# Optimization experiments

Measured on AMD Instinct MI355X. Metric: run time of the kernel, lower is better.

## Reference

```python
import jax, jax.numpy as jnp
import numpy as np

H = 1024          # h_dim
FF = 4 * H
E = 8             # num_expert
TOP_K = 2


def setup_inputs() -> dict:
    key = jax.random.key(0)
    ks = jax.random.split(key, 7)
    B, S = 4, 2048
    s = 0.02
    return {
        "x": jax.random.normal(ks[0], (B, S, H), dtype=jnp.float32),
        "Wg": jax.random.normal(ks[1], (H, E), dtype=jnp.float32) * s,
        "bg": jnp.zeros((E,), dtype=jnp.float32),
        "W1": jax.random.normal(ks[2], (E, H, FF), dtype=jnp.float32) * s,
        "b1": jnp.zeros((E, FF), dtype=jnp.float32),
        "W2": jax.random.normal(ks[3], (E, FF, H), dtype=jnp.float32) * s,
        "b2": jnp.zeros((E, H), dtype=jnp.float32),
    }


def _moe(x, Wg, bg, W1, b1, W2, b2):
    B, S, h = x.shape
    hs = x.reshape(-1, h)                                  # [T, H]
    logits = hs @ Wg + bg                                  # [T, E]
    probs = jax.nn.softmax(logits.astype(jnp.float32), axis=-1)
    w, idx = jax.lax.top_k(probs, TOP_K)                   # [T, K]
    w = jax.nn.softmax(w, axis=-1).astype(x.dtype)         # renormalize over top-k
    out = jnp.zeros_like(hs)
    for e in range(E):
        # per-token combine weight for expert e (0 if not selected)
        w_e = jnp.sum(w * (idx == e), axis=-1)             # [T]
        y = jax.nn.relu(hs @ W1[e] + b1[e]) @ W2[e] + b2[e]  # [T, H]
        out = out + w_e[:, None] * y
    return out.reshape(B, S, h), logits


def reference(x, Wg, bg, W1, b1, W2, b2):
    return _moe(x, Wg, bg, W1, b1, W2, b2)
```

## Files before the change

### kernel.cpp

```cpp
#include <hip/hip_runtime.h>
#include <hip/hip_bf16.h>

#define T_TOKENS 8192
#define HD 1024
#define FF 4096
#define NEXP 8
#define NR_MAX 17408

typedef __attribute__((ext_vector_type(8))) short bf16x8;
typedef __attribute__((ext_vector_type(4))) float f32x4;
typedef unsigned short ushort8v __attribute__((ext_vector_type(8)));

static __device__ __forceinline__ float b2f(ushort u) {
    union { unsigned u; float f; } c; c.u = ((unsigned)u) << 16; return c.f;
}
static __device__ __forceinline__ ushort f2b(float f) {
    union { float f; unsigned u; } c; c.f = f;
    unsigned r = c.u + 0x7fffu + ((c.u >> 16) & 1u);
    return (ushort)(r >> 16);
}

__global__ __launch_bounds__(256) void gate_kernel(
    const float* __restrict__ x, const float* __restrict__ Wg, const float* __restrict__ bg,
    float* __restrict__ logits, int* __restrict__ counts,
    int* __restrict__ e0a, int* __restrict__ e1a,
    float* __restrict__ w0a, float* __restrict__ w1a)
{
    int t = blockIdx.x * 4 + (threadIdx.x >> 6);
    int l = threadIdx.x & 63;
    const float* xr = x + (size_t)t * HD;
    float acc[8] = {0,0,0,0,0,0,0,0};
    #pragma unroll
    for (int i = 0; i < 4; ++i) {
        int h0 = i * 256 + l * 4;
        float4 xv = *(const float4*)(xr + h0);
        #pragma unroll
        for (int j = 0; j < 4; ++j) {
            float xs = (&xv.x)[j];
            const float4* wr = (const float4*)(Wg + (size_t)(h0 + j) * NEXP);
            float4 wa = wr[0], wb = wr[1];
            acc[0] = fmaf(xs, wa.x, acc[0]);
            acc[1] = fmaf(xs, wa.y, acc[1]);
            acc[2] = fmaf(xs, wa.z, acc[2]);
            acc[3] = fmaf(xs, wa.w, acc[3]);
            acc[4] = fmaf(xs, wb.x, acc[4]);
            acc[5] = fmaf(xs, wb.y, acc[5]);
            acc[6] = fmaf(xs, wb.z, acc[6]);
            acc[7] = fmaf(xs, wb.w, acc[7]);
        }
    }
    #pragma unroll
    for (int off = 32; off > 0; off >>= 1) {
        #pragma unroll
        for (int e = 0; e < 8; ++e) acc[e] += __shfl_down(acc[e], off, 64);
    }
    if (l == 0) {
        float lg[8];
        #pragma unroll
        for (int e = 0; e < 8; ++e) {
            lg[e] = acc[e] + bg[e];
            logits[(size_t)t * NEXP + e] = lg[e];
        }
        float m = lg[0];
        #pragma unroll
        for (int e = 1; e < 8; ++e) m = fmaxf(m, lg[e]);
        float p[8], s = 0.f;
        #pragma unroll
        for (int e = 0; e < 8; ++e) { p[e] = expf(lg[e] - m); s += p[e]; }
        float inv = 1.f / s;
        #pragma unroll
        for (int e = 0; e < 8; ++e) p[e] *= inv;
        int i0 = 0;
        #pragma unroll
        for (int e = 1; e < 8; ++e) if (p[e] > p[i0]) i0 = e;
        int i1 = (i0 == 0) ? 1 : 0;
        #pragma unroll
        for (int e = 0; e < 8; ++e) if (e != i0 && p[e] > p[i1]) i1 = e;
        float ed = expf(p[i1] - p[i0]);
        float w0 = 1.f / (1.f + ed);
        float w1 = ed / (1.f + ed);
        e0a[t] = i0; e1a[t] = i1; w0a[t] = w0; w1a[t] = w1;
        atomicAdd(&counts[i0], 1);
        atomicAdd(&counts[i1], 1);
    }
}

__global__ void offsets_kernel(const int* __restrict__ counts, int* __restrict__ off) {
    if (threadIdx.x == 0) {
        int o = 0;
        for (int e = 0; e < 8; ++e) { off[e] = o; o += (counts[e] + 127) & ~127; }
        off[8] = o;
    }
}

__global__ __launch_bounds__(256) void assign_kernel(
    const int* __restrict__ e0a, const int* __restrict__ e1a,
    const int* __restrict__ off, int* __restrict__ fill,
    int* __restrict__ row0, int* __restrict__ row1, int* __restrict__ row_token)
{
    int t = blockIdx.x * 256 + threadIdx.x;
    if (t >= T_TOKENS) return;
    int e0 = e0a[t];
    int r0 = off[e0] + atomicAdd(&fill[e0], 1);
    row0[t] = r0; row_token[r0] = t;
    int e1 = e1a[t];
    int r1 = off[e1] + atomicAdd(&fill[e1], 1);
    row1[t] = r1; row_token[r1] = t;
}

__global__ __launch_bounds__(256) void gather_kernel(
    const float* __restrict__ x, const int* __restrict__ row_token, ushort* __restrict__ Xp)
{
    int r = blockIdx.x;
    int tok = row_token[r];
    int c = threadIdx.x * 4;
    ushort4 o;
    if (tok >= 0 && tok < T_TOKENS) {
        float4 v = *(const float4*)(x + (size_t)tok * HD + c);
        o.x = f2b(v.x); o.y = f2b(v.y); o.z = f2b(v.z); o.w = f2b(v.w);
    } else {
        o.x = 0; o.y = 0; o.z = 0; o.w = 0;
    }
    *(ushort4*)(Xp + (size_t)r * HD + c) = o;
}

__global__ __launch_bounds__(256) void transpose_cvt_kernel(
    const float* __restrict__ in, ushort* __restrict__ out, int R, int C)
{
    __shared__ ushort tile[64][65];
    size_t esz = (size_t)R * C;
    const float* ein = in + (size_t)blockIdx.z * esz;
    ushort* eout = out + (size_t)blockIdx.z * esz;
    int c0 = blockIdx.x * 64, r0 = blockIdx.y * 64;
    int tr = threadIdx.x >> 4;
    int tc = (threadIdx.x & 15) * 4;
    #pragma unroll
    for (int i = 0; i < 4; ++i) {
        int r = tr + i * 16;
        float4 v = *(const float4*)(ein + (size_t)(r0 + r) * C + c0 + tc);
        tile[r][tc + 0] = f2b(v.x);
        tile[r][tc + 1] = f2b(v.y);
        tile[r][tc + 2] = f2b(v.z);
        tile[r][tc + 3] = f2b(v.w);
    }
    __syncthreads();
    int twc = threadIdx.x >> 3;
    int twr = (threadIdx.x & 7) * 8;
    #pragma unroll
    for (int i = 0; i < 2; ++i) {
        int cc = twc + i * 32;
        ushort8v v;
        #pragma unroll
        for (int j = 0; j < 8; ++j) v[j] = tile[twr + j][cc];
        *(ushort8v*)(eout + (size_t)(c0 + cc) * R + r0 + twr) = v;
    }
}

template<int K, int NTOT, bool RELU, bool NTSTORE>
__global__ __launch_bounds__(256) void gemm_kernel(
    const ushort* __restrict__ A, const ushort* __restrict__ Bt,
    const float* __restrict__ bias, ushort* __restrict__ Out,
    const int* __restrict__ off)
{
    constexpr int NT = NTOT / 128;
    __shared__ __align__(16) ushort lds[2][2][128 * 32];

    int nwg = gridDim.x;
    int bid = blockIdx.x;
    int wgid = (bid & 7) * (nwg >> 3) + (bid >> 3);
    int ntile = wgid % NT;
    int mtile = wgid / NT;
    int r0 = mtile * 128;
    int total = off[8];
    if (r0 >= total) return;
    int e = 0;
    #pragma unroll
    for (int q = 0; q < 7; ++q) if (r0 >= off[q + 1]) e = q + 1;

    int tid = threadIdx.x;
    int w = tid >> 6, lane = tid & 63;
    int wr = w >> 1, wc = w & 1;
    int lr = lane & 15, lk = lane >> 4;

    const ushort* Ab = A + (size_t)r0 * K;
    const ushort* Bb = Bt + ((size_t)e * NTOT + (size_t)ntile * 128) * K;

    auto stage = [&](const ushort* gbase, ushort* ldsbase) {
        #pragma unroll
        for (int issue = 0; issue < 2; ++issue) {
            int row = issue * 64 + w * 16 + (lane >> 2);
            int chunk = (lane & 3) ^ ((lane >> 3) & 3);
            const ushort* g = gbase + (size_t)row * K + chunk * 8;
            ushort* lp = ldsbase + (issue * 64 + w * 16) * 32;
            __builtin_amdgcn_global_load_lds(
                (const __attribute__((address_space(1))) void*)g,
                (__attribute__((address_space(3))) void*)lp, 16, 0, 0);
        }
    };

    stage(Ab, &lds[0][0][0]);
    stage(Bb, &lds[0][1][0]);

    f32x4 acc[4][4];
    #pragma unroll
    for (int mi = 0; mi < 4; ++mi)
        #pragma unroll
        for (int ni = 0; ni < 4; ++ni) acc[mi][ni] = (f32x4){0.f, 0.f, 0.f, 0.f};

    __syncthreads();

    constexpr int KT = K / 32;
    int cur = 0;
    int slot = lk ^ ((lr >> 1) & 3);
    for (int kt = 0; kt < KT; ++kt) {
        if (kt + 1 < KT) {
            stage(Ab + (kt + 1) * 32, &lds[cur ^ 1][0][0]);
            stage(Bb + (kt + 1) * 32, &lds[cur ^ 1][1][0]);
        }
        const ushort* As = &lds[cur][0][0];
        const ushort* Bs = &lds[cur][1][0];
        bf16x8 a[4], b[4];
        #pragma unroll
        for (int mi = 0; mi < 4; ++mi)
            a[mi] = *(const bf16x8*)(As + (wr * 64 + mi * 16 + lr) * 32 + slot * 8);
        #pragma unroll
        for (int ni = 0; ni < 4; ++ni)
            b[ni] = *(const bf16x8*)(Bs + (wc * 64 + ni * 16 + lr) * 32 + slot * 8);
        #pragma unroll
        for (int mi = 0; mi < 4; ++mi)
            #pragma unroll
            for (int ni = 0; ni < 4; ++ni)
                acc[mi][ni] = __builtin_amdgcn_mfma_f32_16x16x32_bf16(
                    a[mi], b[ni], acc[mi][ni], 0, 0, 0);
        __syncthreads();
        cur ^= 1;
    }

    int c0 = ntile * 128 + wc * 64;
    int rbase = r0 + wr * 64;
    #pragma unroll
    for (int ni = 0; ni < 4; ++ni) {
        int n = c0 + ni * 16 + lr;
        float bv = bias[(size_t)e * NTOT + n];
        #pragma unroll
        for (int mi = 0; mi < 4; ++mi) {
            int m = rbase + mi * 16 + lk * 4;
            #pragma unroll
            for (int j = 0; j < 4; ++j) {
                float v = acc[mi][ni][j] + bv;
                if (RELU) v = fmaxf(v, 0.f);
                ushort* p = &Out[(size_t)(m + j) * NTOT + n];
                if (NTSTORE) __builtin_nontemporal_store(f2b(v), p);
                else *p = f2b(v);
            }
        }
    }
}

__global__ __launch_bounds__(256) void combine_kernel(
    const ushort* __restrict__ Y, const int* __restrict__ row0, const int* __restrict__ row1,
    const float* __restrict__ w0a, const float* __restrict__ w1a, float* __restrict__ out)
{
    int t = blockIdx.x;
    int c = threadIdx.x * 4;
    int r0 = row0[t], r1 = row1[t];
    float w0 = w0a[t], w1 = w1a[t];
    ushort4 ya = *(const ushort4*)(Y + (size_t)r0 * HD + c);
    ushort4 yb = *(const ushort4*)(Y + (size_t)r1 * HD + c);
    float4 o;
    o.x = w0 * b2f(ya.x) + w1 * b2f(yb.x);
    o.y = w0 * b2f(ya.y) + w1 * b2f(yb.y);
    o.z = w0 * b2f(ya.z) + w1 * b2f(yb.z);
    o.w = w0 * b2f(ya.w) + w1 * b2f(yb.w);
    *(float4*)(out + (size_t)t * HD + c) = o;
}

#define WSA(x) (((x) + 255) & ~(size_t)255)
static constexpr size_t OFF_COUNTS = 0;
static constexpr size_t OFF_FILL   = 64;
static constexpr size_t OFF_OFF    = 128;
static constexpr size_t OFF_E0     = 256;
static constexpr size_t OFF_E1     = OFF_E0 + (size_t)T_TOKENS * 4;
static constexpr size_t OFF_W0     = OFF_E1 + (size_t)T_TOKENS * 4;
static constexpr size_t OFF_W1A    = OFF_W0 + (size_t)T_TOKENS * 4;
static constexpr size_t OFF_R0     = OFF_W1A + (size_t)T_TOKENS * 4;
static constexpr size_t OFF_R1     = OFF_R0 + (size_t)T_TOKENS * 4;
static constexpr size_t OFF_RT     = OFF_R1 + (size_t)T_TOKENS * 4;
static constexpr size_t OFF_XP     = WSA(OFF_RT + (size_t)NR_MAX * 4);
static constexpr size_t OFF_W1T    = OFF_XP  + (size_t)NR_MAX * HD * 2;
static constexpr size_t OFF_W2T    = OFF_W1T + (size_t)NEXP * FF * HD * 2;
static constexpr size_t OFF_H1     = OFF_W2T + (size_t)NEXP * HD * FF * 2;
static constexpr size_t OFF_Y      = OFF_H1  + (size_t)NR_MAX * FF * 2;
static constexpr size_t WS_NEEDED  = OFF_Y   + (size_t)NR_MAX * HD * 2;

extern "C" void kernel_launch(void* const* d_in, const int* in_sizes, int n_in,
                              void* d_out, int out_size, void* d_ws, size_t ws_size,
                              hipStream_t stream) {
    (void)in_sizes; (void)n_in; (void)out_size;
    const float* x  = (const float*)d_in[0];
    const float* Wg = (const float*)d_in[1];
    const float* bg = (const float*)d_in[2];
    const float* W1 = (const float*)d_in[3];
    const float* b1 = (const float*)d_in[4];
    const float* W2 = (const float*)d_in[5];
    const float* b2 = (const float*)d_in[6];
    float* out    = (float*)d_out;
    float* logits = out + (size_t)T_TOKENS * HD;

    if (ws_size < WS_NEEDED) return;

    char* ws = (char*)d_ws;
    int*    counts = (int*)(ws + OFF_COUNTS);
    int*    fill   = (int*)(ws + OFF_FILL);
    int*    offp   = (int*)(ws + OFF_OFF);
    int*    e0a    = (int*)(ws + OFF_E0);
    int*    e1a    = (int*)(ws + OFF_E1);
    float*  w0a    = (float*)(ws + OFF_W0);
    float*  w1a    = (float*)(ws + OFF_W1A);
    int*    row0   = (int*)(ws + OFF_R0);
    int*    row1   = (int*)(ws + OFF_R1);
    int*    rowtok = (int*)(ws + OFF_RT);
    ushort* Xp     = (ushort*)(ws + OFF_XP);
    ushort* W1T    = (ushort*)(ws + OFF_W1T);
    ushort* W2T    = (ushort*)(ws + OFF_W2T);
    ushort* H1     = (ushort*)(ws + OFF_H1);
    ushort* Y      = (ushort*)(ws + OFF_Y);

    hipMemsetAsync(ws, 0, 256, stream);
    hipMemsetAsync(rowtok, 0xFF, (size_t)NR_MAX * 4, stream);

    gate_kernel<<<T_TOKENS / 4, 256, 0, stream>>>(x, Wg, bg, logits, counts, e0a, e1a, w0a, w1a);
    offsets_kernel<<<1, 64, 0, stream>>>(counts, offp);
    assign_kernel<<<T_TOKENS / 256, 256, 0, stream>>>(e0a, e1a, offp, fill, row0, row1, rowtok);
    gather_kernel<<<NR_MAX, 256, 0, stream>>>(x, rowtok, Xp);
    transpose_cvt_kernel<<<dim3(FF / 64, HD / 64, NEXP), 256, 0, stream>>>(W1, W1T, HD, FF);
    transpose_cvt_kernel<<<dim3(HD / 64, FF / 64, NEXP), 256, 0, stream>>>(W2, W2T, FF, HD);
    gemm_kernel<HD, FF, true, true>
        <<<(FF / 128) * (NR_MAX / 128), 256, 0, stream>>>(Xp, W1T, b1, H1, offp);
    gemm_kernel<FF, HD, false, false>
        <<<(HD / 128) * (NR_MAX / 128), 256, 0, stream>>>(H1, W2T, b2, Y, offp);
    combine_kernel<<<T_TOKENS, 256, 0, stream>>>(Y, row0, row1, w0a, w1a, out);
}
```

Baseline: 820.4 us.

## Fuse offsets into assign, merge weight transposes, remap GEMM tiles

Folds the single-thread offsets kernel into the assign kernel, which now computes offsets per block in shared memory. It also merges the two weight transpose-convert launches into one, widens the gather to 8 elements per thread, adds an occupancy hint to the GEMM, and uses an M-fast tile mapping for the first GEMM. The nontemporal store on H1 is dropped. Together these aim to cut launch count and improve L2 reuse of the weight tiles, at the cost of a float LDS tile in the transpose (more shared memory) and possibly more register pressure from the launch bound.

Result: faster. 772.5 us (-5.8%).

```diff
diff --git a/kernel.cpp b/kernel.cpp
--- a/kernel.cpp
+++ b/kernel.cpp
@@ -85,19 +85,23 @@
     }
 }
 
-__global__ void offsets_kernel(const int* __restrict__ counts, int* __restrict__ off) {
+__global__ __launch_bounds__(256) void assign_kernel(
+    const int* __restrict__ e0a, const int* __restrict__ e1a,
+    const int* __restrict__ counts, int* __restrict__ fill, int* __restrict__ offg,
+    int* __restrict__ row0, int* __restrict__ row1, int* __restrict__ row_token)
+{
+    __shared__ int off[9];
     if (threadIdx.x == 0) {
         int o = 0;
+        #pragma unroll
         for (int e = 0; e < 8; ++e) { off[e] = o; o += (counts[e] + 127) & ~127; }
         off[8] = o;
-    }
-}
-
-__global__ __launch_bounds__(256) void assign_kernel(
-    const int* __restrict__ e0a, const int* __restrict__ e1a,
-    const int* __restrict__ off, int* __restrict__ fill,
-    int* __restrict__ row0, int* __restrict__ row1, int* __restrict__ row_token)
-{
+        if (blockIdx.x == 0) {
+            #pragma unroll
+            for (int i = 0; i < 9; ++i) offg[i] = off[i];
+        }
+    }
+    __syncthreads();
     int t = blockIdx.x * 256 + threadIdx.x;
     if (t >= T_TOKENS) return;
     int e0 = e0a[t];
@@ -111,53 +115,67 @@
 __global__ __launch_bounds__(256) void gather_kernel(
     const float* __restrict__ x, const int* __restrict__ row_token, ushort* __restrict__ Xp)
 {
-    int r = blockIdx.x;
+    int r = blockIdx.x * 2 + (threadIdx.x >> 7);
+    int c = (threadIdx.x & 127) * 8;
     int tok = row_token[r];
-    int c = threadIdx.x * 4;
-    ushort4 o;
+    ushort8v o;
     if (tok >= 0 && tok < T_TOKENS) {
-        float4 v = *(const float4*)(x + (size_t)tok * HD + c);
-        o.x = f2b(v.x); o.y = f2b(v.y); o.z = f2b(v.z); o.w = f2b(v.w);
+        const float* src = x + (size_t)tok * HD + c;
+        float4 v1 = *(const float4*)(src);
+        float4 v2 = *(const float4*)(src + 4);
+        o[0] = f2b(v1.x); o[1] = f2b(v1.y); o[2] = f2b(v1.z); o[3] = f2b(v1.w);
+        o[4] = f2b(v2.x); o[5] = f2b(v2.y); o[6] = f2b(v2.z); o[7] = f2b(v2.w);
     } else {
-        o.x = 0; o.y = 0; o.z = 0; o.w = 0;
-    }
-    *(ushort4*)(Xp + (size_t)r * HD + c) = o;
-}
-
-__global__ __launch_bounds__(256) void transpose_cvt_kernel(
-    const float* __restrict__ in, ushort* __restrict__ out, int R, int C)
-{
-    __shared__ ushort tile[64][65];
-    size_t esz = (size_t)R * C;
-    const float* ein = in + (size_t)blockIdx.z * esz;
-    ushort* eout = out + (size_t)blockIdx.z * esz;
-    int c0 = blockIdx.x * 64, r0 = blockIdx.y * 64;
+        o = (ushort8v){0,0,0,0,0,0,0,0};
+    }
+    *(ushort8v*)(Xp + (size_t)r * HD + c) = o;
+}
+
+__global__ __launch_bounds__(256) void transpose_cvt_all(
+    const float* __restrict__ W1, const float* __restrict__ W2,
+    ushort* __restrict__ W1T, ushort* __restrict__ W2T)
+{
+    __shared__ float tile[64][65];
+    int b = blockIdx.x;
+    const float* in; ushort* out; int R, C, tid2, clog;
+    if (b < 8192) {
+        int e = b >> 10; tid2 = b & 1023;
+        in = W1 + (size_t)e * HD * FF; out = W1T + (size_t)e * HD * FF;
+        R = HD; C = FF; clog = 6;
+    } else {
+        int bb = b - 8192; int e = bb >> 10; tid2 = bb & 1023;
+        in = W2 + (size_t)e * FF * HD; out = W2T + (size_t)e * FF * HD;
+        R = FF; C = HD; clog = 4;
+    }
+    int rt = tid2 >> clog, ct = tid2 & ((1 << clog) - 1);
+    int r0 = rt * 64, c0 = ct * 64;
+
     int tr = threadIdx.x >> 4;
     int tc = (threadIdx.x & 15) * 4;
     #pragma unroll
     for (int i = 0; i < 4; ++i) {
         int r = tr + i * 16;
-        float4 v = *(const float4*)(ein + (size_t)(r0 + r) * C + c0 + tc);
-        tile[r][tc + 0] = f2b(v.x);
-        tile[r][tc + 1] = f2b(v.y);
-        tile[r][tc + 2] = f2b(v.z);
-        tile[r][tc + 3] = f2b(v.w);
+        float4 v = *(const float4*)(in + (size_t)(r0 + r) * C + c0 + tc);
+        tile[r][tc + 0] = v.x;
+        tile[r][tc + 1] = v.y;
+        tile[r][tc + 2] = v.z;
+        tile[r][tc + 3] = v.w;
     }
     __syncthreads();
-    int twc = threadIdx.x >> 3;
-    int twr = (threadIdx.x & 7) * 8;
+    int cc = threadIdx.x >> 3;
+    int rr = (threadIdx.x & 7) * 8;
     #pragma unroll
     for (int i = 0; i < 2; ++i) {
-        int cc = twc + i * 32;
-        ushort8v v;
-        #pragma unroll
-        for (int j = 0; j < 8; ++j) v[j] = tile[twr + j][cc];
-        *(ushort8v*)(eout + (size_t)(c0 + cc) * R + r0 + twr) = v;
-    }
-}
-
-template<int K, int NTOT, bool RELU, bool NTSTORE>
-__global__ __launch_bounds__(256) void gemm_kernel(
+        int c = cc + i * 32;
+        ushort8v o;
+        #pragma unroll
+        for (int j = 0; j < 8; ++j) o[j] = f2b(tile[rr + j][c]);
+        *(ushort8v*)(out + (size_t)(c0 + c) * R + r0 + rr) = o;
+    }
+}
+
+template<int K, int NTOT, bool RELU, bool MFAST>
+__global__ __launch_bounds__(256, 4) void gemm_kernel(
     const ushort* __restrict__ A, const ushort* __restrict__ Bt,
     const float* __restrict__ bias, ushort* __restrict__ Out,
     const int* __restrict__ off)
@@ -166,16 +184,24 @@
     __shared__ __align__(16) ushort lds[2][2][128 * 32];
 
     int nwg = gridDim.x;
-    int bid = blockIdx.x;
-    int wgid = (bid & 7) * (nwg >> 3) + (bid >> 3);
-    int ntile = wgid % NT;
-    int mtile = wgid / NT;
+    int chunkc = nwg >> 3;
+    int cid = blockIdx.x & 7, q = blockIdx.x >> 3;
+    int mtile, ntile;
+    if constexpr (MFAST) {
+        int mloc = chunkc / NT;
+        mtile = cid * mloc + q % mloc;
+        ntile = q / mloc;
+    } else {
+        int wgid = cid * chunkc + q;
+        ntile = wgid % NT;
+        mtile = wgid / NT;
+    }
     int r0 = mtile * 128;
     int total = off[8];
     if (r0 >= total) return;
     int e = 0;
     #pragma unroll
-    for (int q = 0; q < 7; ++q) if (r0 >= off[q + 1]) e = q + 1;
+    for (int qq = 0; qq < 7; ++qq) if (r0 >= off[qq + 1]) e = qq + 1;
 
     int tid = threadIdx.x;
     int w = tid >> 6, lane = tid & 63;
@@ -249,9 +275,7 @@
             for (int j = 0; j < 4; ++j) {
                 float v = acc[mi][ni][j] + bv;
                 if (RELU) v = fmaxf(v, 0.f);
-                ushort* p = &Out[(size_t)(m + j) * NTOT + n];
-                if (NTSTORE) __builtin_nontemporal_store(f2b(v), p);
-                else *p = f2b(v);
+                Out[(size_t)(m + j) * NTOT + n] = f2b(v);
             }
         }
     }
@@ -330,11 +354,9 @@
     hipMemsetAsync(rowtok, 0xFF, (size_t)NR_MAX * 4, stream);
 
     gate_kernel<<<T_TOKENS / 4, 256, 0, stream>>>(x, Wg, bg, logits, counts, e0a, e1a, w0a, w1a);
-    offsets_kernel<<<1, 64, 0, stream>>>(counts, offp);
-    assign_kernel<<<T_TOKENS / 256, 256, 0, stream>>>(e0a, e1a, offp, fill, row0, row1, rowtok);
-    gather_kernel<<<NR_MAX, 256, 0, stream>>>(x, rowtok, Xp);
-    transpose_cvt_kernel<<<dim3(FF / 64, HD / 64, NEXP), 256, 0, stream>>>(W1, W1T, HD, FF);
-    transpose_cvt_kernel<<<dim3(HD / 64, FF / 64, NEXP), 256, 0, stream>>>(W2, W2T, FF, HD);
+    assign_kernel<<<T_TOKENS / 256, 256, 0, stream>>>(e0a, e1a, counts, fill, offp, row0, row1, rowtok);
+    gather_kernel<<<NR_MAX / 2, 256, 0, stream>>>(x, rowtok, Xp);
+    transpose_cvt_all<<<8192 + 8192, 256, 0, stream>>>(W1, W2, W1T, W2T);
     gemm_kernel<HD, FF, true, true>
         <<<(FF / 128) * (NR_MAX / 128), 256, 0, stream>>>(Xp, W1T, b1, H1, offp);
     gemm_kernel<FF, HD, false, false>
```
